# Kernel optimization log

Hardware: AMD Instinct MI355X
Metric: run time of the kernel (lower is better)

Reference implementation:

```python
import jax, jax.numpy as jnp
import numpy as np

N_NODES = 50000
N_EDGES = 1600000
NFEAT, NHID, NCLASS = 512, 128, 40


def setup_inputs() -> dict:
    key = jax.random.key(0)
    ks = jax.random.split(key, 10)
    x = jax.random.normal(ks[0], (N_NODES, NFEAT), dtype=jnp.float32)
    edge_src = jax.random.randint(ks[1], (N_EDGES,), 0, N_NODES, dtype=jnp.int32)
    edge_dst = jax.random.randint(ks[2], (N_EDGES,), 0, N_NODES, dtype=jnp.int32)
    edge_weight = jax.random.uniform(ks[3], (N_EDGES,), dtype=jnp.float32)
    # GraphConvolution params: gc1 (nfeat->nhid), one additional (nhid->nhid), gc2 (nhid->nclass)
    s1 = 1.0 / np.sqrt(NHID)
    s2 = 1.0 / np.sqrt(NCLASS)
    W1 = jax.random.uniform(ks[4], (NFEAT, NHID), minval=-s1, maxval=s1, dtype=jnp.float32)
    b1 = jax.random.uniform(ks[5], (NHID,), minval=-s1, maxval=s1, dtype=jnp.float32)
    Wh = jax.random.uniform(ks[6], (NHID, NHID), minval=-s1, maxval=s1, dtype=jnp.float32)
    bh = jax.random.uniform(ks[7], (NHID,), minval=-s1, maxval=s1, dtype=jnp.float32)
    W2 = jax.random.uniform(ks[8], (NHID, NCLASS), minval=-s2, maxval=s2, dtype=jnp.float32)
    b2 = jax.random.uniform(ks[9], (NCLASS,), minval=-s2, maxval=s2, dtype=jnp.float32)
    return {"x": x, "edge_src": edge_src, "edge_dst": edge_dst, "edge_weight": edge_weight,
            "W1": W1, "b1": b1, "Wh": Wh, "bh": bh, "W2": W2, "b2": b2}


def reference(x, edge_src, edge_dst, edge_weight, W1, b1, Wh, bh, W2, b2):
    def spmm(h):
        # out[i] = sum_j adj[i, j] * h[j]  with adj given as weighted edge list (src=j, dst=i)
        return jax.ops.segment_sum(edge_weight[:, None] * h[edge_src], edge_dst,
                                   num_segments=x.shape[0])

    def gconv(h, W, b):
        return spmm(h @ W) + b  # dense transform then sparse aggregation

    h = jax.nn.relu(gconv(x, W1, b1))       # gc1
    h = jax.nn.relu(gconv(h, Wh, bh))        # additional hidden layer
    h = gconv(h, W2, b2)                     # gc2
    return jax.nn.log_softmax(h, axis=1)
```

## Files before the change

### kernel.cpp

```cpp
#include <hip/hip_runtime.h>
#include <hip/hip_bf16.h>
#include <math.h>

#define N_NODES 50000
#define N_EDGES 1600000
#define NFEAT 512
#define NHID 128
#define NCLASS 40

#define NBUCKETS 196
#define BUCKET_CAP 16384

typedef __attribute__((ext_vector_type(8))) short bf16x8;
typedef __attribute__((ext_vector_type(4))) float f32x4;

static __device__ __forceinline__ float asfloat_u32(unsigned int u) {
    union { unsigned int u; float f; } c;
    c.u = u;
    return c.f;
}
static __device__ __forceinline__ unsigned int asu32_f(float f) {
    union { float f; unsigned int u; } c;
    c.f = f;
    return c.u;
}
static __device__ __forceinline__ unsigned short f2bf(float f) {
    union { float f; unsigned int u; } c;
    c.f = f;
    unsigned int r = c.u + 0x7FFFu + ((c.u >> 16) & 1u);
    return (unsigned short)(r >> 16);
}

__global__ __launch_bounds__(256) void prep_kernel(const float* __restrict__ W1,
                                                   unsigned short* __restrict__ Wt1,
                                                   const float* __restrict__ Wh,
                                                   unsigned short* __restrict__ Wth,
                                                   const float* __restrict__ W2,
                                                   unsigned short* __restrict__ Wt2,
                                                   int* __restrict__ bucketCursor) {
    int idx = blockIdx.x * 256 + threadIdx.x;
    if (idx < NFEAT * NHID) {
        int k = idx >> 7;
        int n = idx & 127;
        Wt1[(size_t)n * NFEAT + k] = f2bf(W1[idx]);
    } else if (idx < NFEAT * NHID + NHID * NHID) {
        int j = idx - NFEAT * NHID;
        int k = j >> 7;
        int n = j & 127;
        Wth[(size_t)n * NHID + k] = f2bf(Wh[j]);
    } else if (idx < NFEAT * NHID + NHID * NHID + 64 * NHID) {
        int j = idx - (NFEAT * NHID + NHID * NHID);
        int n = j & 63;
        int k = j >> 6;
        Wt2[(size_t)n * NHID + k] = (n < NCLASS) ? f2bf(W2[(size_t)k * NCLASS + n]) : 0;
    } else {
        int j = idx - (NFEAT * NHID + NHID * NHID + 64 * NHID);
        if (j < NBUCKETS) bucketCursor[j] = j * BUCKET_CAP;
    }
}

#define LDPB 72
#define GEMM_LDS_BYTES (2 * 128 * LDPB * 2)

template <bool A_IS_BF16>
static __device__ __forceinline__ void gemm64_body(const void* __restrict__ Ap,
                                                   const unsigned short* __restrict__ Wt,
                                                   unsigned short* __restrict__ C,
                                                   const int M, const int K,
                                                   char* smem, int bid) {
    unsigned short* Bs0 = (unsigned short*)smem;
    unsigned short* Bs1 = (unsigned short*)smem + 128 * LDPB;
    const int tid = threadIdx.x;
    const int wave = tid >> 6;
    const int lane = tid & 63;
    const int ln = lane & 15;
    const int quad = lane >> 4;
    const int row0 = bid * 64;

    const int arow = row0 + wave * 16 + ln;
    const bool aOk = arow < M;
    const unsigned short* Abf = (const unsigned short*)Ap + (size_t)arow * K + quad * 8;
    const float* Af = (const float*)Ap + (size_t)arow * K + quad * 8;

    const int bn = tid >> 1;
    const int bk = (tid & 1) * 32;
    const unsigned short* Bg = Wt + (size_t)bn * K + bk;

    const int NK = K >> 6;

    f32x4 acc[8];
#pragma unroll
    for (int t = 0; t < 8; ++t) acc[t] = (f32x4){0.f, 0.f, 0.f, 0.f};

    bf16x8 qb0, qb1, qb2, qb3;
    bf16x8 pva0, pva1;
    float4 pf0, pf1, pf2, pf3;

#define GV2_LOAD_A(kc)                                                       \
    do {                                                                     \
        if (A_IS_BF16) {                                                     \
            if (aOk) {                                                       \
                pva0 = *(const bf16x8*)(Abf + (kc));                         \
                pva1 = *(const bf16x8*)(Abf + (kc) + 32);                    \
            }                                                                \
        } else {                                                             \
            if (aOk) {                                                       \
                pf0 = *(const float4*)(Af + (kc));                           \
                pf1 = *(const float4*)(Af + (kc) + 4);                       \
                pf2 = *(const float4*)(Af + (kc) + 32);                      \
                pf3 = *(const float4*)(Af + (kc) + 36);                      \
            }                                                                \
        }                                                                    \
    } while (0)

#define GV2_LOAD_B(kc)                                                       \
    do {                                                                     \
        qb0 = *(const bf16x8*)(Bg + (kc));                                   \
        qb1 = *(const bf16x8*)(Bg + (kc) + 8);                               \
        qb2 = *(const bf16x8*)(Bg + (kc) + 16);                              \
        qb3 = *(const bf16x8*)(Bg + (kc) + 24);                              \
    } while (0)

#define GV2_STORE_B(Bdst)                                                    \
    do {                                                                     \
        *(bf16x8*)&(Bdst)[bn * LDPB + bk] = qb0;                             \
        *(bf16x8*)&(Bdst)[bn * LDPB + bk + 8] = qb1;                         \
        *(bf16x8*)&(Bdst)[bn * LDPB + bk + 16] = qb2;                        \
        *(bf16x8*)&(Bdst)[bn * LDPB + bk + 24] = qb3;                        \
    } while (0)

    GV2_LOAD_B(0);
    GV2_STORE_B(Bs0);
    GV2_LOAD_A(0);
    if (NK > 1) GV2_LOAD_B(64);
    __syncthreads();

    for (int i = 0; i < NK; ++i) {
        unsigned short* Bcur = (i & 1) ? Bs1 : Bs0;
        unsigned short* Bnxt = (i & 1) ? Bs0 : Bs1;

        bf16x8 a0, a1;
        if (A_IS_BF16) {
            if (aOk) {
                a0 = pva0;
                a1 = pva1;
            } else {
#pragma unroll
                for (int j = 0; j < 8; ++j) { a0[j] = 0; a1[j] = 0; }
            }
        } else {
            if (aOk) {
                a0[0] = (short)f2bf(pf0.x); a0[1] = (short)f2bf(pf0.y);
                a0[2] = (short)f2bf(pf0.z); a0[3] = (short)f2bf(pf0.w);
                a0[4] = (short)f2bf(pf1.x); a0[5] = (short)f2bf(pf1.y);
                a0[6] = (short)f2bf(pf1.z); a0[7] = (short)f2bf(pf1.w);
                a1[0] = (short)f2bf(pf2.x); a1[1] = (short)f2bf(pf2.y);
                a1[2] = (short)f2bf(pf2.z); a1[3] = (short)f2bf(pf2.w);
                a1[4] = (short)f2bf(pf3.x); a1[5] = (short)f2bf(pf3.y);
                a1[6] = (short)f2bf(pf3.z); a1[7] = (short)f2bf(pf3.w);
            } else {
#pragma unroll
                for (int j = 0; j < 8; ++j) { a0[j] = 0; a1[j] = 0; }
            }
        }
        if (i + 1 < NK) GV2_LOAD_A((i + 1) * 64);

#pragma unroll
        for (int t = 0; t < 8; ++t) {
            bf16x8 b0 = *(const bf16x8*)&Bcur[(t * 16 + ln) * LDPB + quad * 8];
            acc[t] = __builtin_amdgcn_mfma_f32_16x16x32_bf16(a0, b0, acc[t], 0, 0, 0);
        }
#pragma unroll
        for (int t = 0; t < 8; ++t) {
            bf16x8 b1 = *(const bf16x8*)&Bcur[(t * 16 + ln) * LDPB + 32 + quad * 8];
            acc[t] = __builtin_amdgcn_mfma_f32_16x16x32_bf16(a1, b1, acc[t], 0, 0, 0);
        }

        if (i + 1 < NK) {
            GV2_STORE_B(Bnxt);
            if (i + 2 < NK) GV2_LOAD_B((i + 2) * 64);
        }
        __syncthreads();
    }

#undef GV2_LOAD_A
#undef GV2_LOAD_B
#undef GV2_STORE_B

#pragma unroll
    for (int t = 0; t < 8; ++t) {
#pragma unroll
        for (int r = 0; r < 4; ++r) {
            int row = row0 + wave * 16 + quad * 4 + r;
            if (row < M) C[(size_t)row * 128 + t * 16 + ln] = f2bf(acc[t][r]);
        }
    }
}

static __device__ __forceinline__ void bin_body(const int* __restrict__ src,
                                                const int* __restrict__ dst,
                                                const float* __restrict__ w,
                                                int* __restrict__ bucketCursor,
                                                uint2* __restrict__ binned,
                                                int n, char* smem, int bid) {
    uint2* recs = (uint2*)smem;
    int* hist = (int*)(smem + 32768);
    int* lincl = hist + 256;
    int* gbase = lincl + 256;
    int* cur = gbase + 256;
    const int tid = threadIdx.x;
    const int wave = tid >> 6;
    const int lane = tid & 63;
    const int base = bid * 4096;

    hist[tid] = 0;
    __syncthreads();
#pragma unroll
    for (int r = 0; r < 16; ++r) {
        int e = base + r * 256 + tid;
        if (e < n) atomicAdd(&hist[dst[e] >> 8], 1);
    }
    __syncthreads();
    int v = hist[tid];
    lincl[tid] = v;
    __syncthreads();
    for (int off = 1; off < 256; off <<= 1) {
        int t = (tid >= off) ? lincl[tid - off] : 0;
        __syncthreads();
        lincl[tid] += t;
        __syncthreads();
    }
    if (tid < NBUCKETS && v > 0) gbase[tid] = atomicAdd(&bucketCursor[tid], v);
    cur[tid] = lincl[tid] - v;
    __syncthreads();
#pragma unroll
    for (int r = 0; r < 16; ++r) {
        int e = base + r * 256 + tid;
        if (e < n) {
            int d = dst[e];
            int pos = atomicAdd(&cur[d >> 8], 1);
            uint2 rec;
            rec.x = (unsigned int)src[e] | ((unsigned int)(d & 255) << 16);
            rec.y = asu32_f(w[e]);
            recs[pos] = rec;
        }
    }
    __syncthreads();
    for (int B = wave; B < NBUCKETS; B += 4) {
        int cnt = hist[B];
        if (cnt == 0) continue;
        int lst = lincl[B] - cnt;
        int g = gbase[B];
        for (int i = lane; i < cnt; i += 64) binned[g + i] = recs[lst + i];
    }
}

#define GEMM1_BLOCKS 782
#define BIN_BLOCKS 391
__global__ __launch_bounds__(256) void fused_gemm1_bin(const float* __restrict__ x,
                                                       const unsigned short* __restrict__ Wt1,
                                                       unsigned short* __restrict__ tb,
                                                       const int* __restrict__ src,
                                                       const int* __restrict__ dst,
                                                       const float* __restrict__ w,
                                                       int* __restrict__ bucketCursor,
                                                       uint2* __restrict__ binned) {
    __shared__ char smem[GEMM_LDS_BYTES];
    if (blockIdx.x < GEMM1_BLOCKS) {
        gemm64_body<false>(x, Wt1, tb, N_NODES, NFEAT, smem, blockIdx.x);
    } else {
        bin_body(src, dst, w, bucketCursor, binned, N_EDGES, smem,
                 blockIdx.x - GEMM1_BLOCKS);
    }
}

__global__ __launch_bounds__(256) void gemm64_l2(const unsigned short* __restrict__ A,
                                                 const unsigned short* __restrict__ Wt,
                                                 unsigned short* __restrict__ C) {
    __shared__ char smem[GEMM_LDS_BYTES];
    gemm64_body<true>(A, Wt, C, N_NODES, NHID, smem, blockIdx.x);
}

__global__ __launch_bounds__(1024) void build_csr(const uint2* __restrict__ binned,
                                                  const int* __restrict__ bucketCursor,
                                                  unsigned int* __restrict__ pairs,
                                                  int* __restrict__ row_ptr) {
    __shared__ int bs[256];
    __shared__ int hist[256];
    __shared__ int sc[256];
    __shared__ int cur[256];
    const int b = blockIdx.x;
    const int tid = threadIdx.x;

    if (tid < 256) bs[tid] = (tid < NBUCKETS) ? (bucketCursor[tid] - tid * BUCKET_CAP) : 0;
    if (tid < 256) hist[tid] = 0;
    __syncthreads();
    for (int off = 1; off < 256; off <<= 1) {
        int t = 0;
        if (tid < 256 && tid >= off) t = bs[tid - off];
        __syncthreads();
        if (tid < 256) bs[tid] += t;
        __syncthreads();
    }
    const int cnt = bucketCursor[b] - b * BUCKET_CAP;
    const int segStart = bs[b] - cnt;
    if (b == NBUCKETS - 1 && tid == 0) row_ptr[N_NODES] = bs[NBUCKETS - 1];
    const uint2* seg = binned + (size_t)b * BUCKET_CAP;

    for (int i = tid; i < cnt; i += 1024)
        atomicAdd(&hist[seg[i].x >> 16], 1);
    __syncthreads();
    if (tid < 256) {
        int v = hist[tid];
        sc[tid] = v;
    }
    __syncthreads();
    for (int off = 1; off < 256; off <<= 1) {
        int t = 0;
        if (tid < 256 && tid >= off) t = sc[tid - off];
        __syncthreads();
        if (tid < 256) sc[tid] += t;
        __syncthreads();
    }
    if (tid < 256) {
        int excl = sc[tid] - hist[tid];
        int node = b * 256 + tid;
        if (node < N_NODES) row_ptr[node] = segStart + excl;
        cur[tid] = segStart + excl;
    }
    __syncthreads();
    for (int i = tid; i < cnt; i += 1024) {
        uint2 p = seg[i];
        int pos = atomicAdd(&cur[p.x >> 16], 1);
        pairs[pos] = (p.x & 0xFFFFu) | ((unsigned int)f2bf(asfloat_u32(p.y)) << 16);
    }
}

#define LDP2 136
__global__ __launch_bounds__(256) void gemm_n64(const unsigned short* __restrict__ A,
                                                const unsigned short* __restrict__ Wt2,
                                                unsigned short* __restrict__ C, int M) {
    __shared__ unsigned short As[64 * LDP2];
    __shared__ unsigned short Bs[64 * LDP2];
    const int tid = threadIdx.x;
    const int wave = tid >> 6;
    const int lane = tid & 63;
    const int ln = lane & 15;
    const int quad = lane >> 4;
    const int row0 = blockIdx.x * 64;

#pragma unroll
    for (int i = 0; i < 4; ++i) {
        int q = tid + 256 * i;
        int r = q >> 4;
        int c = (q & 15) * 8;
        bf16x8 v;
        if (row0 + r < M) {
            v = *(const bf16x8*)(A + (size_t)(row0 + r) * 128 + c);
        } else {
#pragma unroll
            for (int j = 0; j < 8; ++j) v[j] = 0;
        }
        *(bf16x8*)&As[r * LDP2 + c] = v;
    }
#pragma unroll
    for (int i = 0; i < 4; ++i) {
        int q = tid + 256 * i;
        int r = q >> 4;
        int c = (q & 15) * 8;
        *(bf16x8*)&Bs[r * LDP2 + c] = *(const bf16x8*)(Wt2 + (size_t)r * 128 + c);
    }
    __syncthreads();

    f32x4 acc[4];
#pragma unroll
    for (int t = 0; t < 4; ++t) acc[t] = (f32x4){0.f, 0.f, 0.f, 0.f};

#pragma unroll
    for (int kc = 0; kc < 128; kc += 32) {
        bf16x8 a = *(const bf16x8*)&As[(wave * 16 + ln) * LDP2 + kc + quad * 8];
#pragma unroll
        for (int t = 0; t < 4; ++t) {
            bf16x8 b = *(const bf16x8*)&Bs[(t * 16 + ln) * LDP2 + kc + quad * 8];
            acc[t] = __builtin_amdgcn_mfma_f32_16x16x32_bf16(a, b, acc[t], 0, 0, 0);
        }
    }

#pragma unroll
    for (int t = 0; t < 4; ++t) {
#pragma unroll
        for (int r = 0; r < 4; ++r) {
            int row = row0 + wave * 16 + quad * 4 + r;
            if (row < M) C[(size_t)row * 64 + t * 16 + ln] = f2bf(acc[t][r]);
        }
    }
}

__global__ __launch_bounds__(256) void spmm_bias_relu_bf16(const unsigned short* __restrict__ t,
                                                           const int* __restrict__ row_ptr,
                                                           const unsigned int* __restrict__ pairs,
                                                           const float* __restrict__ bias,
                                                           unsigned short* __restrict__ out) {
    const int node = blockIdx.x * 4 + (threadIdx.x >> 6);
    const int lane = threadIdx.x & 63;
    const int g = lane >> 4;
    const int fl = (lane & 15) * 8;
    const int e0 = row_ptr[node];
    const int e1 = row_ptr[node + 1];
    float acc8[8];
#pragma unroll
    for (int j = 0; j < 8; ++j) acc8[j] = 0.f;

    int e = e0;
    for (; e + 32 <= e1; e += 32) {
        unsigned int p[8];
        uint4 v[8];
#pragma unroll
        for (int i = 0; i < 8; ++i) p[i] = pairs[e + 4 * i + g];
#pragma unroll
        for (int i = 0; i < 8; ++i)
            v[i] = *(const uint4*)(t + (size_t)(p[i] & 0xFFFFu) * 128 + fl);
#pragma unroll
        for (int i = 0; i < 8; ++i) {
            float w = asfloat_u32(p[i] & 0xFFFF0000u);
            acc8[0] += w * asfloat_u32(v[i].x << 16);
            acc8[1] += w * asfloat_u32(v[i].x & 0xFFFF0000u);
            acc8[2] += w * asfloat_u32(v[i].y << 16);
            acc8[3] += w * asfloat_u32(v[i].y & 0xFFFF0000u);
            acc8[4] += w * asfloat_u32(v[i].z << 16);
            acc8[5] += w * asfloat_u32(v[i].z & 0xFFFF0000u);
            acc8[6] += w * asfloat_u32(v[i].w << 16);
            acc8[7] += w * asfloat_u32(v[i].w & 0xFFFF0000u);
        }
    }
    for (; e + 4 <= e1; e += 4) {
        unsigned int p = pairs[e + g];
        uint4 v = *(const uint4*)(t + (size_t)(p & 0xFFFFu) * 128 + fl);
        float w = asfloat_u32(p & 0xFFFF0000u);
        acc8[0] += w * asfloat_u32(v.x << 16);
        acc8[1] += w * asfloat_u32(v.x & 0xFFFF0000u);
        acc8[2] += w * asfloat_u32(v.y << 16);
        acc8[3] += w * asfloat_u32(v.y & 0xFFFF0000u);
        acc8[4] += w * asfloat_u32(v.z << 16);
        acc8[5] += w * asfloat_u32(v.z & 0xFFFF0000u);
        acc8[6] += w * asfloat_u32(v.w << 16);
        acc8[7] += w * asfloat_u32(v.w & 0xFFFF0000u);
    }
    if (g < e1 - e) {
        unsigned int p = pairs[e + g];
        uint4 v = *(const uint4*)(t + (size_t)(p & 0xFFFFu) * 128 + fl);
        float w = asfloat_u32(p & 0xFFFF0000u);
        acc8[0] += w * asfloat_u32(v.x << 16);
        acc8[1] += w * asfloat_u32(v.x & 0xFFFF0000u);
        acc8[2] += w * asfloat_u32(v.y << 16);
        acc8[3] += w * asfloat_u32(v.y & 0xFFFF0000u);
        acc8[4] += w * asfloat_u32(v.z << 16);
        acc8[5] += w * asfloat_u32(v.z & 0xFFFF0000u);
        acc8[6] += w * asfloat_u32(v.w << 16);
        acc8[7] += w * asfloat_u32(v.w & 0xFFFF0000u);
    }
#pragma unroll
    for (int j = 0; j < 8; ++j) {
        acc8[j] += __shfl_xor(acc8[j], 16);
        acc8[j] += __shfl_xor(acc8[j], 32);
    }
    if (g == 0) {
        float4 b0 = *(const float4*)&bias[fl];
        float4 b1 = *(const float4*)&bias[fl + 4];
        acc8[0] = fmaxf(acc8[0] + b0.x, 0.f);
        acc8[1] = fmaxf(acc8[1] + b0.y, 0.f);
        acc8[2] = fmaxf(acc8[2] + b0.z, 0.f);
        acc8[3] = fmaxf(acc8[3] + b0.w, 0.f);
        acc8[4] = fmaxf(acc8[4] + b1.x, 0.f);
        acc8[5] = fmaxf(acc8[5] + b1.y, 0.f);
        acc8[6] = fmaxf(acc8[6] + b1.z, 0.f);
        acc8[7] = fmaxf(acc8[7] + b1.w, 0.f);
        uint4 o;
        o.x = ((unsigned int)f2bf(acc8[0])) | (((unsigned int)f2bf(acc8[1])) << 16);
        o.y = ((unsigned int)f2bf(acc8[2])) | (((unsigned int)f2bf(acc8[3])) << 16);
        o.z = ((unsigned int)f2bf(acc8[4])) | (((unsigned int)f2bf(acc8[5])) << 16);
        o.w = ((unsigned int)f2bf(acc8[6])) | (((unsigned int)f2bf(acc8[7])) << 16);
        *(uint4*)(out + (size_t)node * 128 + fl) = o;
    }
}

__global__ __launch_bounds__(256) void spmm_logsoftmax(const unsigned short* __restrict__ t,
                                                       const int* __restrict__ row_ptr,
                                                       const unsigned int* __restrict__ pairs,
                                                       const float* __restrict__ bias,
                                                       float* __restrict__ out) {
    const int node = blockIdx.x * 4 + (threadIdx.x >> 6);
    const int lane = threadIdx.x & 63;
    const int g = lane >> 4;
    const int fe = (lane & 15) * 4;
    const int e0 = row_ptr[node];
    const int e1 = row_ptr[node + 1];
    float a0 = 0.f, a1 = 0.f, a2 = 0.f, a3 = 0.f;
    int e = e0;
    for (; e + 32 <= e1; e += 32) {
        unsigned int p[8];
        uint2 v[8];
#pragma unroll
        for (int i = 0; i < 8; ++i) p[i] = pairs[e + 4 * i + g];
#pragma unroll
        for (int i = 0; i < 8; ++i)
            v[i] = *(const uint2*)(t + (size_t)(p[i] & 0xFFFFu) * 64 + fe);
#pragma unroll
        for (int i = 0; i < 8; ++i) {
            float w = asfloat_u32(p[i] & 0xFFFF0000u);
            a0 += w * asfloat_u32(v[i].x << 16);
            a1 += w * asfloat_u32(v[i].x & 0xFFFF0000u);
            a2 += w * asfloat_u32(v[i].y << 16);
            a3 += w * asfloat_u32(v[i].y & 0xFFFF0000u);
        }
    }
    for (; e + 4 <= e1; e += 4) {
        unsigned int p = pairs[e + g];
        uint2 v = *(const uint2*)(t + (size_t)(p & 0xFFFFu) * 64 + fe);
        float w = asfloat_u32(p & 0xFFFF0000u);
        a0 += w * asfloat_u32(v.x << 16);
        a1 += w * asfloat_u32(v.x & 0xFFFF0000u);
        a2 += w * asfloat_u32(v.y << 16);
        a3 += w * asfloat_u32(v.y & 0xFFFF0000u);
    }
    if (g < e1 - e) {
        unsigned int p = pairs[e + g];
        uint2 v = *(const uint2*)(t + (size_t)(p & 0xFFFFu) * 64 + fe);
        float w = asfloat_u32(p & 0xFFFF0000u);
        a0 += w * asfloat_u32(v.x << 16);
        a1 += w * asfloat_u32(v.x & 0xFFFF0000u);
        a2 += w * asfloat_u32(v.y << 16);
        a3 += w * asfloat_u32(v.y & 0xFFFF0000u);
    }
    a0 += __shfl_xor(a0, 16); a0 += __shfl_xor(a0, 32);
    a1 += __shfl_xor(a1, 16); a1 += __shfl_xor(a1, 32);
    a2 += __shfl_xor(a2, 16); a2 += __shfl_xor(a2, 32);
    a3 += __shfl_xor(a3, 16); a3 += __shfl_xor(a3, 32);

    const bool valid = (lane & 15) < 10;
    float l0 = -INFINITY, l1 = -INFINITY, l2 = -INFINITY, l3 = -INFINITY;
    if (valid) {
        float4 b = *(const float4*)&bias[fe];
        l0 = a0 + b.x; l1 = a1 + b.y; l2 = a2 + b.z; l3 = a3 + b.w;
    }
    float m = fmaxf(fmaxf(l0, l1), fmaxf(l2, l3));
#pragma unroll
    for (int off = 8; off; off >>= 1) m = fmaxf(m, __shfl_xor(m, off));
    float s = valid ? (__expf(l0 - m) + __expf(l1 - m) + __expf(l2 - m) + __expf(l3 - m)) : 0.f;
#pragma unroll
    for (int off = 8; off; off >>= 1) s += __shfl_xor(s, off);
    if (valid && g == 0) {
        float ls = __logf(s);
        float4 o;
        o.x = l0 - m - ls; o.y = l1 - m - ls; o.z = l2 - m - ls; o.w = l3 - m - ls;
        *(float4*)&out[(size_t)node * NCLASS + fe] = o;
    }
}


extern "C" void kernel_launch(void* const* d_in, const int* in_sizes, int n_in,
                              void* d_out, int out_size, void* d_ws, size_t ws_size,
                              hipStream_t stream) {
    const float* x = (const float*)d_in[0];
    const int* edge_src = (const int*)d_in[1];
    const int* edge_dst = (const int*)d_in[2];
    const float* edge_weight = (const float*)d_in[3];
    const float* W1 = (const float*)d_in[4];
    const float* b1 = (const float*)d_in[5];
    const float* Wh = (const float*)d_in[6];
    const float* bh = (const float*)d_in[7];
    const float* W2 = (const float*)d_in[8];
    const float* b2 = (const float*)d_in[9];
    float* out = (float*)d_out;

    size_t off = 0;
    auto carve = [&](size_t bytes) {
        void* p = (char*)d_ws + off;
        off += (bytes + 511) & ~(size_t)511;
        return p;
    };
    unsigned short* tb = (unsigned short*)carve((size_t)N_NODES * 128 * 2);
    unsigned short* hb = (unsigned short*)carve((size_t)N_NODES * 128 * 2);
    unsigned short* t3 = (unsigned short*)carve((size_t)N_NODES * 64 * 2);
    unsigned short* Wt1 = (unsigned short*)carve((size_t)NFEAT * NHID * 2);
    unsigned short* Wth = (unsigned short*)carve((size_t)NHID * NHID * 2);
    unsigned short* Wt2 = (unsigned short*)carve((size_t)64 * NHID * 2);
    int* row_ptr = (int*)carve((size_t)(N_NODES + 4) * 4);
    int* bucketCursor = (int*)carve((size_t)NBUCKETS * 4);
    uint2* binned = (uint2*)carve((size_t)NBUCKETS * BUCKET_CAP * 8);
    unsigned int* pairs = (unsigned int*)carve((size_t)N_EDGES * 4);
    (void)ws_size; (void)n_in; (void)in_sizes; (void)out_size;

    const int prepBlocks =
        (NFEAT * NHID + NHID * NHID + 64 * NHID + NBUCKETS + 255) / 256;
    const int spmmBlocks = N_NODES / 4;
    const int gemmBlocks = (N_NODES + 63) / 64;

    prep_kernel<<<prepBlocks, 256, 0, stream>>>(W1, Wt1, Wh, Wth, W2, Wt2, bucketCursor);

    fused_gemm1_bin<<<GEMM1_BLOCKS + BIN_BLOCKS, 256, 0, stream>>>(
        x, Wt1, tb, edge_src, edge_dst, edge_weight, bucketCursor, binned);

    build_csr<<<NBUCKETS, 1024, 0, stream>>>(binned, bucketCursor, pairs, row_ptr);

    spmm_bias_relu_bf16<<<spmmBlocks, 256, 0, stream>>>(tb, row_ptr, pairs, b1, hb);

    gemm64_l2<<<gemmBlocks, 256, 0, stream>>>(hb, Wth, tb);
    spmm_bias_relu_bf16<<<spmmBlocks, 256, 0, stream>>>(tb, row_ptr, pairs, bh, hb);

    gemm_n64<<<gemmBlocks, 256, 0, stream>>>(hb, Wt2, t3, N_NODES);
    spmm_logsoftmax<<<spmmBlocks, 256, 0, stream>>>(t3, row_ptr, pairs, b2, out);
}
```

Before: 386.4 us.

## Store dense transform outputs in FP8 and simplify GEMM and binning

The intermediate H·W results for the first two layers are now written in FP8 e4m3 instead of bf16, which halves the gather traffic in the two SpMM passes; those passes dequantize with the hardware packed-convert builtins when available. The GEMM body drops its double-buffered B tile and register prefetch for a single LDS buffer with two barriers per k-step. The binning pass stops staging records in LDS and scatters them straight to global memory. FP8 loses a lot of precision and may hurt accuracy, and the simpler GEMM and binning give up latency hiding and write coalescing.

```diff
diff --git a/kernel.cpp b/kernel.cpp
--- a/kernel.cpp
+++ b/kernel.cpp
@@ -1,5 +1,6 @@
 #include <hip/hip_runtime.h>
 #include <hip/hip_bf16.h>
+#include <hip/hip_fp8.h>
 #include <math.h>
 
 #define N_NODES 50000
@@ -13,6 +14,7 @@
 
 typedef __attribute__((ext_vector_type(8))) short bf16x8;
 typedef __attribute__((ext_vector_type(4))) float f32x4;
+typedef __attribute__((ext_vector_type(2))) float f32x2;
 
 static __device__ __forceinline__ float asfloat_u32(unsigned int u) {
     union { unsigned int u; float f; } c;
@@ -29,6 +31,32 @@
     c.f = f;
     unsigned int r = c.u + 0x7FFFu + ((c.u >> 16) & 1u);
     return (unsigned short)(r >> 16);
+}
+
+static __device__ __forceinline__ float fp8_to_f32_sw(unsigned int x) {
+    float m = asfloat_u32((x & 0x7Fu) << 20) * 0x1p+120f;
+    return asfloat_u32(asu32_f(m) | ((x & 0x80u) << 24));
+}
+static __device__ __forceinline__ void dq4(unsigned int u, float* f) {
+#if __has_builtin(__builtin_amdgcn_cvt_pk_f32_fp8)
+    f32x2 lo = __builtin_amdgcn_cvt_pk_f32_fp8(u, false);
+    f32x2 hi = __builtin_amdgcn_cvt_pk_f32_fp8(u, true);
+    f[0] = lo[0]; f[1] = lo[1]; f[2] = hi[0]; f[3] = hi[1];
+#else
+    f[0] = fp8_to_f32_sw(u & 0xFFu);
+    f[1] = fp8_to_f32_sw((u >> 8) & 0xFFu);
+    f[2] = fp8_to_f32_sw((u >> 16) & 0xFFu);
+    f[3] = fp8_to_f32_sw((u >> 24) & 0xFFu);
+#endif
+}
+static __device__ __forceinline__ unsigned char f2fp8(float f) {
+#if __has_builtin(__builtin_amdgcn_cvt_pk_fp8_f32)
+    int v = __builtin_amdgcn_cvt_pk_fp8_f32(f, f, 0, false);
+    return (unsigned char)(v & 0xFF);
+#else
+    __hip_fp8_e4m3 h(f);
+    return (unsigned char)h.__x;
+#endif
 }
 
 __global__ __launch_bounds__(256) void prep_kernel(const float* __restrict__ W1,
@@ -60,16 +88,15 @@
 }
 
 #define LDPB 72
-#define GEMM_LDS_BYTES (2 * 128 * LDPB * 2)
-
-template <bool A_IS_BF16>
+#define GEMM_LDS_BYTES (128 * LDPB * 2)
+
+template <bool A_IS_BF16, bool OUT_FP8>
 static __device__ __forceinline__ void gemm64_body(const void* __restrict__ Ap,
                                                    const unsigned short* __restrict__ Wt,
-                                                   unsigned short* __restrict__ C,
+                                                   void* __restrict__ Cv,
                                                    const int M, const int K,
                                                    char* smem, int bid) {
-    unsigned short* Bs0 = (unsigned short*)smem;
-    unsigned short* Bs1 = (unsigned short*)smem + 128 * LDPB;
+    unsigned short* Bs = (unsigned short*)smem;
     const int tid = threadIdx.x;
     const int wave = tid >> 6;
     const int lane = tid & 63;
@@ -86,113 +113,83 @@
     const int bk = (tid & 1) * 32;
     const unsigned short* Bg = Wt + (size_t)bn * K + bk;
 
-    const int NK = K >> 6;
-
     f32x4 acc[8];
 #pragma unroll
     for (int t = 0; t < 8; ++t) acc[t] = (f32x4){0.f, 0.f, 0.f, 0.f};
 
-    bf16x8 qb0, qb1, qb2, qb3;
-    bf16x8 pva0, pva1;
-    float4 pf0, pf1, pf2, pf3;
-
-#define GV2_LOAD_A(kc)                                                       \
-    do {                                                                     \
-        if (A_IS_BF16) {                                                     \
-            if (aOk) {                                                       \
-                pva0 = *(const bf16x8*)(Abf + (kc));                         \
-                pva1 = *(const bf16x8*)(Abf + (kc) + 32);                    \
-            }                                                                \
-        } else {                                                             \
-            if (aOk) {                                                       \
-                pf0 = *(const float4*)(Af + (kc));                           \
-                pf1 = *(const float4*)(Af + (kc) + 4);                       \
-                pf2 = *(const float4*)(Af + (kc) + 32);                      \
-                pf3 = *(const float4*)(Af + (kc) + 36);                      \
-            }                                                                \
-        }                                                                    \
-    } while (0)
-
-#define GV2_LOAD_B(kc)                                                       \
-    do {                                                                     \
-        qb0 = *(const bf16x8*)(Bg + (kc));                                   \
-        qb1 = *(const bf16x8*)(Bg + (kc) + 8);                               \
-        qb2 = *(const bf16x8*)(Bg + (kc) + 16);                              \
-        qb3 = *(const bf16x8*)(Bg + (kc) + 24);                              \
-    } while (0)
-
-#define GV2_STORE_B(Bdst)                                                    \
-    do {                                                                     \
-        *(bf16x8*)&(Bdst)[bn * LDPB + bk] = qb0;                             \
-        *(bf16x8*)&(Bdst)[bn * LDPB + bk + 8] = qb1;                         \
-        *(bf16x8*)&(Bdst)[bn * LDPB + bk + 16] = qb2;                        \
-        *(bf16x8*)&(Bdst)[bn * LDPB + bk + 24] = qb3;                        \
-    } while (0)
-
-    GV2_LOAD_B(0);
-    GV2_STORE_B(Bs0);
-    GV2_LOAD_A(0);
-    if (NK > 1) GV2_LOAD_B(64);
-    __syncthreads();
-
-    for (int i = 0; i < NK; ++i) {
-        unsigned short* Bcur = (i & 1) ? Bs1 : Bs0;
-        unsigned short* Bnxt = (i & 1) ? Bs0 : Bs1;
+    for (int kc = 0; kc < K; kc += 64) {
+        bf16x8 qb0 = *(const bf16x8*)(Bg + kc);
+        bf16x8 qb1 = *(const bf16x8*)(Bg + kc + 8);
+        bf16x8 qb2 = *(const bf16x8*)(Bg + kc + 16);
+        bf16x8 qb3 = *(const bf16x8*)(Bg + kc + 24);
 
         bf16x8 a0, a1;
         if (A_IS_BF16) {
             if (aOk) {
-                a0 = pva0;
-                a1 = pva1;
+                a0 = *(const bf16x8*)(Abf + kc);
+                a1 = *(const bf16x8*)(Abf + kc + 32);
             } else {
 #pragma unroll
                 for (int j = 0; j < 8; ++j) { a0[j] = 0; a1[j] = 0; }
             }
         } else {
             if (aOk) {
-                a0[0] = (short)f2bf(pf0.x); a0[1] = (short)f2bf(pf0.y);
-                a0[2] = (short)f2bf(pf0.z); a0[3] = (short)f2bf(pf0.w);
-                a0[4] = (short)f2bf(pf1.x); a0[5] = (short)f2bf(pf1.y);
-                a0[6] = (short)f2bf(pf1.z); a0[7] = (short)f2bf(pf1.w);
-                a1[0] = (short)f2bf(pf2.x); a1[1] = (short)f2bf(pf2.y);
-                a1[2] = (short)f2bf(pf2.z); a1[3] = (short)f2bf(pf2.w);
-                a1[4] = (short)f2bf(pf3.x); a1[5] = (short)f2bf(pf3.y);
-                a1[6] = (short)f2bf(pf3.z); a1[7] = (short)f2bf(pf3.w);
+                float4 f0 = *(const float4*)(Af + kc);
+                float4 f1 = *(const float4*)(Af + kc + 4);
+                float4 f2 = *(const float4*)(Af + kc + 32);
+                float4 f3 = *(const float4*)(Af + kc + 36);
+                a0[0] = (short)f2bf(f0.x); a0[1] = (short)f2bf(f0.y);
+                a0[2] = (short)f2bf(f0.z); a0[3] = (short)f2bf(f0.w);
+                a0[4] = (short)f2bf(f1.x); a0[5] = (short)f2bf(f1.y);
+                a0[6] = (short)f2bf(f1.z); a0[7] = (short)f2bf(f1.w);
+                a1[0] = (short)f2bf(f2.x); a1[1] = (short)f2bf(f2.y);
+                a1[2] = (short)f2bf(f2.z); a1[3] = (short)f2bf(f2.w);
+                a1[4] = (short)f2bf(f3.x); a1[5] = (short)f2bf(f3.y);
+                a1[6] = (short)f2bf(f3.z); a1[7] = (short)f2bf(f3.w);
             } else {
 #pragma unroll
                 for (int j = 0; j < 8; ++j) { a0[j] = 0; a1[j] = 0; }
             }
         }
-        if (i + 1 < NK) GV2_LOAD_A((i + 1) * 64);
+
+        __syncthreads();
+        *(bf16x8*)&Bs[bn * LDPB + bk] = qb0;
+        *(bf16x8*)&Bs[bn * LDPB + bk + 8] = qb1;
+        *(bf16x8*)&Bs[bn * LDPB + bk + 16] = qb2;
+        *(bf16x8*)&Bs[bn * LDPB + bk + 24] = qb3;
+        __syncthreads();
 
 #pragma unroll
         for (int t = 0; t < 8; ++t) {
-            bf16x8 b0 = *(const bf16x8*)&Bcur[(t * 16 + ln) * LDPB + quad * 8];
+            bf16x8 b0 = *(const bf16x8*)&Bs[(t * 16 + ln) * LDPB + quad * 8];
             acc[t] = __builtin_amdgcn_mfma_f32_16x16x32_bf16(a0, b0, acc[t], 0, 0, 0);
         }
 #pragma unroll
         for (int t = 0; t < 8; ++t) {
-            bf16x8 b1 = *(const bf16x8*)&Bcur[(t * 16 + ln) * LDPB + 32 + quad * 8];
+            bf16x8 b1 = *(const bf16x8*)&Bs[(t * 16 + ln) * LDPB + 32 + quad * 8];
             acc[t] = __builtin_amdgcn_mfma_f32_16x16x32_bf16(a1, b1, acc[t], 0, 0, 0);
         }
-
-        if (i + 1 < NK) {
-            GV2_STORE_B(Bnxt);
-            if (i + 2 < NK) GV2_LOAD_B((i + 2) * 64);
-        }
-        __syncthreads();
-    }
-
-#undef GV2_LOAD_A
-#undef GV2_LOAD_B
-#undef GV2_STORE_B
-
-#pragma unroll
-    for (int t = 0; t < 8; ++t) {
-#pragma unroll
-        for (int r = 0; r < 4; ++r) {
-            int row = row0 + wave * 16 + quad * 4 + r;
-            if (row < M) C[(size_t)row * 128 + t * 16 + ln] = f2bf(acc[t][r]);
+    }
+
+    if (OUT_FP8) {
+        unsigned char* C8 = (unsigned char*)Cv;
+#pragma unroll
+        for (int t = 0; t < 8; ++t) {
+#pragma unroll
+            for (int r = 0; r < 4; ++r) {
+                int row = row0 + wave * 16 + quad * 4 + r;
+                if (row < M) C8[(size_t)row * 128 + t * 16 + ln] = f2fp8(acc[t][r]);
+            }
+        }
+    } else {
+        unsigned short* C = (unsigned short*)Cv;
+#pragma unroll
+        for (int t = 0; t < 8; ++t) {
+#pragma unroll
+            for (int r = 0; r < 4; ++r) {
+                int row = row0 + wave * 16 + quad * 4 + r;
+                if (row < M) C[(size_t)row * 128 + t * 16 + ln] = f2bf(acc[t][r]);
+            }
         }
     }
 }
@@ -203,17 +200,11 @@
                                                 int* __restrict__ bucketCursor,
                                                 uint2* __restrict__ binned,
                                                 int n, char* smem, int bid) {
-    uint2* recs = (uint2*)smem;
-    int* hist = (int*)(smem + 32768);
-    int* lincl = hist + 256;
-    int* gbase = lincl + 256;
-    int* cur = gbase + 256;
+    int* hist = (int*)smem;
+    int* cur = (int*)smem + NBUCKETS;
     const int tid = threadIdx.x;
-    const int wave = tid >> 6;
-    const int lane = tid & 63;
     const int base = bid * 4096;
-
-    hist[tid] = 0;
+    if (tid < NBUCKETS) hist[tid] = 0;
     __syncthreads();
 #pragma unroll
     for (int r = 0; r < 16; ++r) {
@@ -221,17 +212,8 @@
         if (e < n) atomicAdd(&hist[dst[e] >> 8], 1);
     }
     __syncthreads();
-    int v = hist[tid];
-    lincl[tid] = v;
-    __syncthreads();
-    for (int off = 1; off < 256; off <<= 1) {
-        int t = (tid >= off) ? lincl[tid - off] : 0;
-        __syncthreads();
-        lincl[tid] += t;
-        __syncthreads();
-    }
-    if (tid < NBUCKETS && v > 0) gbase[tid] = atomicAdd(&bucketCursor[tid], v);
-    cur[tid] = lincl[tid] - v;
+    if (tid < NBUCKETS && hist[tid] > 0)
+        cur[tid] = atomicAdd(&bucketCursor[tid], hist[tid]);
     __syncthreads();
 #pragma unroll
     for (int r = 0; r < 16; ++r) {
@@ -242,16 +224,8 @@
             uint2 rec;
             rec.x = (unsigned int)src[e] | ((unsigned int)(d & 255) << 16);
             rec.y = asu32_f(w[e]);
-            recs[pos] = rec;
-        }
-    }
-    __syncthreads();
-    for (int B = wave; B < NBUCKETS; B += 4) {
-        int cnt = hist[B];
-        if (cnt == 0) continue;
-        int lst = lincl[B] - cnt;
-        int g = gbase[B];
-        for (int i = lane; i < cnt; i += 64) binned[g + i] = recs[lst + i];
+            binned[pos] = rec;
+        }
     }
 }
 
@@ -259,7 +233,7 @@
 #define BIN_BLOCKS 391
 __global__ __launch_bounds__(256) void fused_gemm1_bin(const float* __restrict__ x,
                                                        const unsigned short* __restrict__ Wt1,
-                                                       unsigned short* __restrict__ tb,
+                                                       unsigned char* __restrict__ tb,
                                                        const int* __restrict__ src,
                                                        const int* __restrict__ dst,
                                                        const float* __restrict__ w,
@@ -267,7 +241,7 @@
                                                        uint2* __restrict__ binned) {
     __shared__ char smem[GEMM_LDS_BYTES];
     if (blockIdx.x < GEMM1_BLOCKS) {
-        gemm64_body<false>(x, Wt1, tb, N_NODES, NFEAT, smem, blockIdx.x);
+        gemm64_body<false, true>(x, Wt1, tb, N_NODES, NFEAT, smem, blockIdx.x);
     } else {
         bin_body(src, dst, w, bucketCursor, binned, N_EDGES, smem,
                  blockIdx.x - GEMM1_BLOCKS);
@@ -276,9 +250,9 @@
 
 __global__ __launch_bounds__(256) void gemm64_l2(const unsigned short* __restrict__ A,
                                                  const unsigned short* __restrict__ Wt,
-                                                 unsigned short* __restrict__ C) {
+                                                 unsigned char* __restrict__ C) {
     __shared__ char smem[GEMM_LDS_BYTES];
-    gemm64_body<true>(A, Wt, C, N_NODES, NHID, smem, blockIdx.x);
+    gemm64_body<true, true>(A, Wt, C, N_NODES, NHID, smem, blockIdx.x);
 }
 
 __global__ __launch_bounds__(1024) void build_csr(const uint2* __restrict__ binned,
@@ -396,11 +370,11 @@
     }
 }
 
-__global__ __launch_bounds__(256) void spmm_bias_relu_bf16(const unsigned short* __restrict__ t,
-                                                           const int* __restrict__ row_ptr,
-                                                           const unsigned int* __restrict__ pairs,
-                                                           const float* __restrict__ bias,
-                                                           unsigned short* __restrict__ out) {
+__global__ __launch_bounds__(256) void spmm_bias_relu_fp8(const unsigned char* __restrict__ t,
+                                                          const int* __restrict__ row_ptr,
+                                                          const unsigned int* __restrict__ pairs,
+                                                          const float* __restrict__ bias,
+                                                          unsigned short* __restrict__ out) {
     const int node = blockIdx.x * 4 + (threadIdx.x >> 6);
     const int lane = threadIdx.x & 63;
     const int g = lane >> 4;
@@ -414,50 +388,41 @@
     int e = e0;
     for (; e + 32 <= e1; e += 32) {
         unsigned int p[8];
-        uint4 v[8];
+        uint2 v[8];
 #pragma unroll
         for (int i = 0; i < 8; ++i) p[i] = pairs[e + 4 * i + g];
 #pragma unroll
         for (int i = 0; i < 8; ++i)
-            v[i] = *(const uint4*)(t + (size_t)(p[i] & 0xFFFFu) * 128 + fl);
+            v[i] = *(const uint2*)(t + (size_t)(p[i] & 0xFFFFu) * 128 + fl);
 #pragma unroll
         for (int i = 0; i < 8; ++i) {
             float w = asfloat_u32(p[i] & 0xFFFF0000u);
-            acc8[0] += w * asfloat_u32(v[i].x << 16);
-            acc8[1] += w * asfloat_u32(v[i].x & 0xFFFF0000u);
-            acc8[2] += w * asfloat_u32(v[i].y << 16);
-            acc8[3] += w * asfloat_u32(v[i].y & 0xFFFF0000u);
-            acc8[4] += w * asfloat_u32(v[i].z << 16);
-            acc8[5] += w * asfloat_u32(v[i].z & 0xFFFF0000u);
-            acc8[6] += w * asfloat_u32(v[i].w << 16);
-            acc8[7] += w * asfloat_u32(v[i].w & 0xFFFF0000u);
+            float f[8];
+            dq4(v[i].x, f);
+            dq4(v[i].y, f + 4);
+#pragma unroll
+            for (int j = 0; j < 8; ++j) acc8[j] += w * f[j];
         }
     }
     for (; e + 4 <= e1; e += 4) {
         unsigned int p = pairs[e + g];
-        uint4 v = *(const uint4*)(t + (size_t)(p & 0xFFFFu) * 128 + fl);
+        uint2 v = *(const uint2*)(t + (size_t)(p & 0xFFFFu) * 128 + fl);
         float w = asfloat_u32(p & 0xFFFF0000u);
-        acc8[0] += w * asfloat_u32(v.x << 16);
-        acc8[1] += w * asfloat_u32(v.x & 0xFFFF0000u);
-        acc8[2] += w * asfloat_u32(v.y << 16);
-        acc8[3] += w * asfloat_u32(v.y & 0xFFFF0000u);
-        acc8[4] += w * asfloat_u32(v.z << 16);
-        acc8[5] += w * asfloat_u32(v.z & 0xFFFF0000u);
-        acc8[6] += w * asfloat_u32(v.w << 16);
-        acc8[7] += w * asfloat_u32(v.w & 0xFFFF0000u);
+        float f[8];
+        dq4(v.x, f);
+        dq4(v.y, f + 4);
+#pragma unroll
+        for (int j = 0; j < 8; ++j) acc8[j] += w * f[j];
     }
     if (g < e1 - e) {
         unsigned int p = pairs[e + g];
-        uint4 v = *(const uint4*)(t + (size_t)(p & 0xFFFFu) * 128 + fl);
+        uint2 v = *(const uint2*)(t + (size_t)(p & 0xFFFFu) * 128 + fl);
         float w = asfloat_u32(p & 0xFFFF0000u);
-        acc8[0] += w * asfloat_u32(v.x << 16);
-        acc8[1] += w * asfloat_u32(v.x & 0xFFFF0000u);
-        acc8[2] += w * asfloat_u32(v.y << 16);
-        acc8[3] += w * asfloat_u32(v.y & 0xFFFF0000u);
-        acc8[4] += w * asfloat_u32(v.z << 16);
-        acc8[5] += w * asfloat_u32(v.z & 0xFFFF0000u);
-        acc8[6] += w * asfloat_u32(v.w << 16);
-        acc8[7] += w * asfloat_u32(v.w & 0xFFFF0000u);
+        float f[8];
+        dq4(v.x, f);
+        dq4(v.y, f + 4);
+#pragma unroll
+        for (int j = 0; j < 8; ++j) acc8[j] += w * f[j];
     }
 #pragma unroll
     for (int j = 0; j < 8; ++j) {
@@ -579,7 +544,7 @@
         off += (bytes + 511) & ~(size_t)511;
         return p;
     };
-    unsigned short* tb = (unsigned short*)carve((size_t)N_NODES * 128 * 2);
+    unsigned char* tb = (unsigned char*)carve((size_t)N_NODES * 128);
     unsigned short* hb = (unsigned short*)carve((size_t)N_NODES * 128 * 2);
     unsigned short* t3 = (unsigned short*)carve((size_t)N_NODES * 64 * 2);
     unsigned short* Wt1 = (unsigned short*)carve((size_t)NFEAT * NHID * 2);
@@ -603,10 +568,10 @@
 
     build_csr<<<NBUCKETS, 1024, 0, stream>>>(binned, bucketCursor, pairs, row_ptr);
 
-    spmm_bias_relu_bf16<<<spmmBlocks, 256, 0, stream>>>(tb, row_ptr, pairs, b1, hb);
+    spmm_bias_relu_fp8<<<spmmBlocks, 256, 0, stream>>>(tb, row_ptr, pairs, b1, hb);
 
     gemm64_l2<<<gemmBlocks, 256, 0, stream>>>(hb, Wth, tb);
-    spmm_bias_relu_bf16<<<spmmBlocks, 256, 0, stream>>>(tb, row_ptr, pairs, bh, hb);
+    spmm_bias_relu_fp8<<<spmmBlocks, 256, 0, stream>>>(tb, row_ptr, pairs, bh, hb);
 
     gemm_n64<<<gemmBlocks, 256, 0, stream>>>(hb, Wt2, t3, N_NODES);
     spmm_logsoftmax<<<spmmBlocks, 256, 0, stream>>>(t3, row_ptr, pairs, b2, out);
```

Result: faster. 360.4 us (-6.7%).
